# Kernel optimization log

Hardware: AMD Instinct MI355X
Metric: run time of the kernel (lower is better)

## Reference

```python
import jax, jax.numpy as jnp
import numpy as np

N_NODES = 16384
N_GRAPHS = 64
NODES_PER_GRAPH = N_NODES // N_GRAPHS
F_IN = 128
E_DIM = 256
N_HEADS = 8
MLP = 1024
N_LAYERS = 4
N_CLASSES = 10
N_EDGES = 262144
LN_EPS = 1e-5


def setup_inputs() -> dict:
    key = jax.random.key(0)
    ks = jax.random.split(key, 32)
    s = 0.02
    inp = {
        "x": jax.random.normal(ks[0], (N_NODES, F_IN), jnp.float32),
        "edge_idx": jax.random.randint(ks[1], (2, N_EDGES), 0, N_NODES, jnp.int32),
        "batch": (jnp.arange(N_NODES, dtype=jnp.int32) // NODES_PER_GRAPH),
        "pos_enc": jax.random.normal(ks[2], (N_NODES, E_DIM), jnp.float32),
        # GCNConv params (torch Linear convention: W is [out, in])
        "gcn_w": jax.random.normal(ks[3], (F_IN, F_IN), jnp.float32) * s,
        "gcn_b": jnp.zeros((F_IN,), jnp.float32),
        "cls": jax.random.normal(ks[4], (E_DIM,), jnp.float32),
        "emb_w": jax.random.normal(ks[5], (E_DIM, F_IN), jnp.float32) * s,
        "emb_b": jnp.zeros((E_DIM,), jnp.float32),
        # stacked transformer-encoder-layer params over L layers
        "in_w": jax.random.normal(ks[6], (N_LAYERS, 3 * E_DIM, E_DIM), jnp.float32) * s,
        "in_b": jnp.zeros((N_LAYERS, 3 * E_DIM), jnp.float32),
        "out_w": jax.random.normal(ks[7], (N_LAYERS, E_DIM, E_DIM), jnp.float32) * s,
        "out_b": jnp.zeros((N_LAYERS, E_DIM), jnp.float32),
        "lin1_w": jax.random.normal(ks[8], (N_LAYERS, MLP, E_DIM), jnp.float32) * s,
        "lin1_b": jnp.zeros((N_LAYERS, MLP), jnp.float32),
        "lin2_w": jax.random.normal(ks[9], (N_LAYERS, E_DIM, MLP), jnp.float32) * s,
        "lin2_b": jnp.zeros((N_LAYERS, E_DIM), jnp.float32),
        "ln1_g": jnp.ones((N_LAYERS, E_DIM), jnp.float32),
        "ln1_beta": jnp.zeros((N_LAYERS, E_DIM), jnp.float32),
        "ln2_g": jnp.ones((N_LAYERS, E_DIM), jnp.float32),
        "ln2_beta": jnp.zeros((N_LAYERS, E_DIM), jnp.float32),
        "fc_w": jax.random.normal(ks[10], (N_CLASSES, E_DIM), jnp.float32) * s,
        "fc_b": jnp.zeros((N_CLASSES,), jnp.float32),
    }
    return inp


def _layer_norm(h, g, b):
    mu = jnp.mean(h, axis=-1, keepdims=True)
    var = jnp.mean(jnp.square(h - mu), axis=-1, keepdims=True)
    return (h - mu) * jax.lax.rsqrt(var + LN_EPS) * g + b


def _gcn_conv(x, edge_idx, gcn_w, gcn_b):
    # PyG GCNConv: lin -> add self-loops -> sym-normalized scatter-add -> +bias
    xw = x @ gcn_w.T                                             # [N, F]
    ar = jnp.arange(N_NODES, dtype=edge_idx.dtype)
    ei = jnp.concatenate([edge_idx, jnp.stack([ar, ar])], axis=1)
    row, col = ei[0], ei[1]
    deg = jax.ops.segment_sum(jnp.ones(ei.shape[1], xw.dtype), col, num_segments=N_NODES)
    dinv = jax.lax.rsqrt(deg)                                    # deg >= 1 (self loops)
    norm = dinv[row] * dinv[col]                                 # [E+N]
    out = jax.ops.segment_sum(norm[:, None] * xw[row], col, num_segments=N_NODES)
    return out + gcn_b


def reference(x, edge_idx, batch, pos_enc, gcn_w, gcn_b, cls, emb_w, emb_b,
              in_w, in_b, out_w, out_b, lin1_w, lin1_b, lin2_w, lin2_b,
              ln1_g, ln1_beta, ln2_g, ln2_beta, fc_w, fc_b):
    h = _gcn_conv(x, edge_idx, gcn_w, gcn_b)
    h = jax.nn.relu(h)
    h = h @ emb_w.T + emb_b + pos_enc                            # [N, E_DIM]
    # batch = arange // NODES_PER_GRAPH (contiguous equal-size graphs):
    # per-graph loop == batched reshape
    h = h.reshape(N_GRAPHS, NODES_PER_GRAPH, E_DIM)
    cls_tok = jnp.broadcast_to(cls, (N_GRAPHS, 1, E_DIM))
    h = jnp.concatenate([cls_tok, h], axis=1)                    # [G, S, E]
    S = NODES_PER_GRAPH + 1
    dh = E_DIM // N_HEADS
    scale = 1.0 / jnp.sqrt(jnp.asarray(dh, h.dtype))
    for l in range(N_LAYERS):
        # post-LN TransformerEncoderLayer (torch default), dropout off
        qkv = jnp.einsum('gse,fe->gsf', h, in_w[l]) + in_b[l]    # [G, S, 3E]
        q, k, v = jnp.split(qkv, 3, axis=-1)
        q = q.reshape(N_GRAPHS, S, N_HEADS, dh).transpose(0, 2, 1, 3)
        k = k.reshape(N_GRAPHS, S, N_HEADS, dh).transpose(0, 2, 1, 3)
        v = v.reshape(N_GRAPHS, S, N_HEADS, dh).transpose(0, 2, 1, 3)
        att = jax.nn.softmax(jnp.einsum('ghqd,ghkd->ghqk', q, k) * scale, axis=-1)
        o = jnp.einsum('ghqk,ghkd->ghqd', att, v)
        o = o.transpose(0, 2, 1, 3).reshape(N_GRAPHS, S, E_DIM)
        o = jnp.einsum('gse,fe->gsf', o, out_w[l]) + out_b[l]
        h = _layer_norm(h + o, ln1_g[l], ln1_beta[l])
        f = jax.nn.relu(jnp.einsum('gse,me->gsm', h, lin1_w[l]) + lin1_b[l])
        f = jnp.einsum('gsm,em->gse', f, lin2_w[l]) + lin2_b[l]
        h = _layer_norm(h + f, ln2_g[l], ln2_beta[l])
    cls_out = h[:, 0, :]                                         # [G, E]
    return cls_out @ fc_w.T + fc_b                               # [G, C]
```

## Files before the change

kernel.cpp:

```cpp
#include <hip/hip_runtime.h>
#include <cstddef>

#define N_NODES 16384
#define N_GRAPHS 64
#define NPG 256
#define F_IN 128
#define E_DIM 256
#define N_HEADS 8
#define DH 32
#define MLP 1024
#define N_LAYERS 4
#define N_CLASSES 10
#define N_EDGES 262144
#define S_LEN 257
#define M_ROWS (N_GRAPHS * S_LEN)
#define M_PAD 16512
#define LN_EPS 1e-5f

typedef __attribute__((ext_vector_type(8))) short bf16x8;
typedef __attribute__((ext_vector_type(4))) float f32x4;

__device__ inline unsigned short f2b1(float f) {
    unsigned u = __float_as_uint(f);
    unsigned r = (u + 0x7fffu + ((u >> 16) & 1u)) >> 16;
    return (unsigned short)r;
}

#define GLOBAL_LOAD_LDS16(g, l) \
    __builtin_amdgcn_global_load_lds((__attribute__((address_space(1))) const void*)(g), \
                                     (__attribute__((address_space(3))) void*)(l), 16, 0, 0)

struct F2BJobs {
    const float* src[7];
    unsigned short* dst[7];
    int n4[7];
};
__global__ __launch_bounds__(256) void f2b_all(F2BJobs jobs) {
#pragma unroll 1
    for (int r = 0; r < 7; ++r) {
        const float4* s = (const float4*)jobs.src[r];
        ushort4* d = (ushort4*)jobs.dst[r];
        const int n4 = jobs.n4[r];
        for (int i = blockIdx.x * 256 + threadIdx.x; i < n4; i += gridDim.x * 256) {
            float4 v = s[i];
            ushort4 o;
            o.x = f2b1(v.x); o.y = f2b1(v.y); o.z = f2b1(v.z); o.w = f2b1(v.w);
            d[i] = o;
        }
    }
}

__global__ __launch_bounds__(256) void gemm_mfma(
    const unsigned short* __restrict__ A, const unsigned short* __restrict__ W,
    const float* __restrict__ bias, const float* __restrict__ add,
    float* __restrict__ outF, unsigned short* __restrict__ outB,
    int M, int N, int K, int relu)
{
    __shared__ __align__(16) unsigned short As[128 * 32];
    __shared__ __align__(16) unsigned short Bs[128 * 32];
    const int tid = threadIdx.x;
    const int wave = tid >> 6;
    const int lane = tid & 63;
    const int bm = blockIdx.y * 128;
    const int bn = blockIdx.x * 128;

    const int srow = (lane >> 2);
    const int scol = (lane & 3) * 8;
    const size_t a_r0 = (size_t)(bm + wave * 16 + srow) * K + scol;
    const size_t b_r0 = (size_t)(bn + wave * 16 + srow) * K + scol;
    unsigned short* ldsA0 = &As[wave * 512];
    unsigned short* ldsA1 = &As[(wave + 4) * 512];
    unsigned short* ldsB0 = &Bs[wave * 512];
    unsigned short* ldsB1 = &Bs[(wave + 4) * 512];

    const int wm = (wave & 1) * 64;
    const int wn = (wave >> 1) * 64;
    const int fr = lane & 15;
    const int fk = (lane >> 4) * 8;

    f32x4 acc[4][4];
#pragma unroll
    for (int i = 0; i < 4; ++i)
#pragma unroll
        for (int j = 0; j < 4; ++j)
            acc[i][j] = (f32x4){0.f, 0.f, 0.f, 0.f};

    for (int k0 = 0; k0 < K; k0 += 32) {
        __syncthreads();
        GLOBAL_LOAD_LDS16(A + a_r0 + k0, ldsA0);
        GLOBAL_LOAD_LDS16(A + a_r0 + (size_t)64 * K + k0, ldsA1);
        GLOBAL_LOAD_LDS16(W + b_r0 + k0, ldsB0);
        GLOBAL_LOAD_LDS16(W + b_r0 + (size_t)64 * K + k0, ldsB1);
        __syncthreads();

        bf16x8 a[4], b[4];
#pragma unroll
        for (int i = 0; i < 4; ++i)
            a[i] = *(const bf16x8*)&As[(wm + i * 16 + fr) * 32 + fk];
#pragma unroll
        for (int j = 0; j < 4; ++j)
            b[j] = *(const bf16x8*)&Bs[(wn + j * 16 + fr) * 32 + fk];
#pragma unroll
        for (int i = 0; i < 4; ++i)
#pragma unroll
            for (int j = 0; j < 4; ++j)
                acc[i][j] = __builtin_amdgcn_mfma_f32_16x16x32_bf16(a[i], b[j], acc[i][j], 0, 0, 0);
    }

    const int er = (lane >> 4) * 4;
    const int ec = lane & 15;
#pragma unroll
    for (int j = 0; j < 4; ++j) {
        const int col = bn + wn + j * 16 + ec;
        const float bs = bias ? bias[col] : 0.f;
#pragma unroll
        for (int i = 0; i < 4; ++i) {
#pragma unroll
            for (int r = 0; r < 4; ++r) {
                const int row = bm + wm + i * 16 + er + r;
                float v = acc[i][j][r] + bs;
                if (add)  v += add[(size_t)row * N + col];
                if (relu) v = fmaxf(v, 0.f);
                if (outF) outF[(size_t)row * N + col] = v;
                if (outB) outB[(size_t)row * N + col] = f2b1(v);
            }
        }
    }
}

__global__ __launch_bounds__(256) void gemm_ln(
    const unsigned short* __restrict__ A, const unsigned short* __restrict__ W,
    const float* __restrict__ bias, const float* __restrict__ g,
    const float* __restrict__ beta,
    float* __restrict__ h, unsigned short* __restrict__ hb, int K)
{
    __shared__ __align__(16) unsigned short As[64 * 32];
    __shared__ __align__(16) unsigned short Bs[256 * 32];
    const int tid  = threadIdx.x;
    const int wave = tid >> 6;
    const int lane = tid & 63;
    const int quad = lane >> 4;
    const int l16  = lane & 15;
    const int bm   = blockIdx.x * 64;

    const int srow = lane >> 2;
    const int scol = (lane & 3) * 8;
    const size_t a_r0 = (size_t)(bm + wave * 16 + srow) * K + scol;
    unsigned short* ldsA = &As[wave * 512];

    f32x4 acc[16];
#pragma unroll
    for (int j = 0; j < 16; ++j) acc[j] = (f32x4){0.f, 0.f, 0.f, 0.f};

    for (int k0 = 0; k0 < K; k0 += 32) {
        __syncthreads();
        GLOBAL_LOAD_LDS16(A + a_r0 + k0, ldsA);
#pragma unroll
        for (int cc = 0; cc < 4; ++cc) {
            const int c = wave + cc * 4;
            GLOBAL_LOAD_LDS16(W + (size_t)(c * 16 + srow) * K + scol + k0, &Bs[c * 512]);
        }
        __syncthreads();
        bf16x8 a = *(const bf16x8*)&As[(wave * 16 + l16) * 32 + quad * 8];
#pragma unroll
        for (int j = 0; j < 16; ++j) {
            bf16x8 b = *(const bf16x8*)&Bs[(j * 16 + l16) * 32 + quad * 8];
            acc[j] = __builtin_amdgcn_mfma_f32_16x16x32_bf16(a, b, acc[j], 0, 0, 0);
        }
    }

    const int row0 = bm + wave * 16 + quad * 4;
    float gv[16], bv[16], biasv[16];
#pragma unroll
    for (int j = 0; j < 16; ++j) {
        const int col = j * 16 + l16;
        gv[j] = g[col]; bv[j] = beta[col]; biasv[j] = bias[col];
    }
#pragma unroll
    for (int r = 0; r < 4; ++r) {
        const int row = row0 + r;
        float v[16];
        float s1 = 0.f, s2 = 0.f;
#pragma unroll
        for (int j = 0; j < 16; ++j) {
            const int col = j * 16 + l16;
            float t = acc[j][r] + biasv[j] + h[(size_t)row * E_DIM + col];
            v[j] = t; s1 += t; s2 += t * t;
        }
        s1 += __shfl_xor(s1, 1, 64); s2 += __shfl_xor(s2, 1, 64);
        s1 += __shfl_xor(s1, 2, 64); s2 += __shfl_xor(s2, 2, 64);
        s1 += __shfl_xor(s1, 4, 64); s2 += __shfl_xor(s2, 4, 64);
        s1 += __shfl_xor(s1, 8, 64); s2 += __shfl_xor(s2, 8, 64);
        const float mu = s1 * (1.f / 256.f);
        const float var = s2 * (1.f / 256.f) - mu * mu;
        const float rstd = rsqrtf(var + LN_EPS);
#pragma unroll
        for (int j = 0; j < 16; ++j) {
            const int col = j * 16 + l16;
            float o = (v[j] - mu) * rstd * gv[j] + bv[j];
            h[(size_t)row * E_DIM + col] = o;
            hb[(size_t)row * E_DIM + col] = f2b1(o);
        }
    }
}

__global__ void deg_count(const int* __restrict__ ei, float* __restrict__ deg) {
    int e = blockIdx.x * blockDim.x + threadIdx.x;
    if (e < N_EDGES) atomicAdd(&deg[ei[N_EDGES + e]], 1.0f);
}

__global__ __launch_bounds__(1024) void scan_deg(const float* __restrict__ deg,
                                                 int* __restrict__ row_start) {
    __shared__ int lds[1024];
    const int t = threadIdx.x;
    const int base = t * 16;
    int loc[16];
    int s = 0;
#pragma unroll
    for (int i = 0; i < 16; ++i) { loc[i] = s; s += (int)deg[base + i]; }
    lds[t] = s;
    __syncthreads();
    for (int off = 1; off < 1024; off <<= 1) {
        int v = lds[t];
        int u = (t >= off) ? lds[t - off] : 0;
        __syncthreads();
        lds[t] = v + u;
        __syncthreads();
    }
    const int excl = (t == 0) ? 0 : lds[t - 1];
#pragma unroll
    for (int i = 0; i < 16; ++i) row_start[base + i] = excl + loc[i];
    if (t == 1023) row_start[16384] = lds[1023];
}

__global__ void make_dinv(float* __restrict__ deg) {
    int i = blockIdx.x * blockDim.x + threadIdx.x;
    if (i < N_NODES) deg[i] = rsqrtf(deg[i] + 1.0f);
}

__global__ void scatter_edges(const int* __restrict__ ei, const float* __restrict__ dinv,
                              const int* __restrict__ row_start, int* __restrict__ cursor,
                              int* __restrict__ esrc, float* __restrict__ enrm) {
    int e = blockIdx.x * 256 + threadIdx.x;
    if (e < N_EDGES) {
        int r = ei[e], c = ei[N_EDGES + e];
        int slot = atomicAdd(&cursor[c], 1);
        int p = row_start[c] + slot;
        esrc[p] = r;
        enrm[p] = dinv[r] * dinv[c];
    }
}

__global__ __launch_bounds__(256) void gcn_gather(
    const float* __restrict__ xw, const int* __restrict__ row_start,
    const int* __restrict__ esrc, const float* __restrict__ enrm,
    const float* __restrict__ dinv, const float* __restrict__ bias,
    unsigned short* __restrict__ aggb) {
    const int n = blockIdx.x * 4 + (threadIdx.x >> 6);
    const int t = threadIdx.x & 63;
    const int e0 = row_start[n], e1 = row_start[n + 1];
    float ax = 0.f, ay = 0.f;
    for (int e = e0; e < e1; ++e) {
        int s = esrc[e];
        float w = enrm[e];
        float2 v = ((const float2*)(xw + (size_t)s * F_IN))[t];
        ax += w * v.x; ay += w * v.y;
    }
    const float di = dinv[n];
    const float w0 = di * di;
    float2 vs = ((const float2*)(xw + (size_t)n * F_IN))[t];
    ax += w0 * vs.x; ay += w0 * vs.y;
    float2 b2 = ((const float2*)bias)[t];
    ushort2 o;
    o.x = f2b1(fmaxf(ax + b2.x, 0.f));
    o.y = f2b1(fmaxf(ay + b2.y, 0.f));
    ((ushort2*)(aggb + (size_t)n * F_IN))[t] = o;
}

__global__ void assemble_h(const float* __restrict__ emb, const float* __restrict__ cls,
                           float* __restrict__ h, unsigned short* __restrict__ hb) {
    int row = blockIdx.x;
    int f = threadIdx.x;
    int g = row / S_LEN, s = row % S_LEN;
    float v = (s == 0) ? cls[f] : emb[((size_t)g * NPG + (s - 1)) * E_DIM + f];
    h[(size_t)row * E_DIM + f] = v;
    hb[(size_t)row * E_DIM + f] = f2b1(v);
}

__global__ __launch_bounds__(256) void attn_mfma(const unsigned short* __restrict__ qkvb,
                                                 unsigned short* __restrict__ ob) {
    const int g  = blockIdx.x >> 3;
    const int hh = blockIdx.x & 7;
    __shared__ __align__(16) unsigned short Ks[272 * 32];
    __shared__ __align__(16) unsigned short VT[32 * 288];
    __shared__ __align__(16) unsigned short Ps[4 * 16 * 288];
    const int tid  = threadIdx.x;
    const int wave = tid >> 6;
    const int lane = tid & 63;
    const int quad = lane >> 4;
    const int l16  = lane & 15;
    const size_t grow0 = (size_t)g * S_LEN;

    for (int s = tid; s < 272; s += 256) {
        uint4* dst = (uint4*)&Ks[s * 32];
        if (s < S_LEN) {
            const uint4* src = (const uint4*)(qkvb + (grow0 + s) * 768 + 256 + hh * 32);
            dst[0] = src[0]; dst[1] = src[1]; dst[2] = src[2]; dst[3] = src[3];
        } else {
            uint4 z = {0u, 0u, 0u, 0u};
            dst[0] = z; dst[1] = z; dst[2] = z; dst[3] = z;
        }
    }
    for (int s = tid; s < 288; s += 256) {
        unsigned short t[32];
        if (s < S_LEN) {
            const uint4* src = (const uint4*)(qkvb + (grow0 + s) * 768 + 512 + hh * 32);
            ((uint4*)t)[0] = src[0]; ((uint4*)t)[1] = src[1];
            ((uint4*)t)[2] = src[2]; ((uint4*)t)[3] = src[3];
        } else {
#pragma unroll
            for (int d = 0; d < 32; ++d) t[d] = 0;
        }
#pragma unroll
        for (int d = 0; d < 32; ++d) VT[d * 288 + s] = t[d];
    }
    unsigned short* Pw = &Ps[wave * 16 * 288];
    for (int i = lane; i < 256; i += 64)
        Pw[(i >> 4) * 288 + 272 + (i & 15)] = 0;
    __syncthreads();

    const float scale = 0.17677669529663687f;
    for (int qt = wave; qt < 17; qt += 4) {
        const int qrow_l = qt * 16 + l16;
        bf16x8 aq = *(const bf16x8*)(qkvb + (grow0 + qrow_l) * 768 + hh * 32 + quad * 8);

        f32x4 sc[17];
#pragma unroll
        for (int kt = 0; kt < 17; ++kt) {
            bf16x8 bk = *(const bf16x8*)&Ks[(kt * 16 + l16) * 32 + quad * 8];
            f32x4 z = (f32x4){0.f, 0.f, 0.f, 0.f};
            sc[kt] = __builtin_amdgcn_mfma_f32_16x16x32_bf16(aq, bk, z, 0, 0, 0);
        }

        float lsum[4] = {0.f, 0.f, 0.f, 0.f};
#pragma unroll
        for (int kt = 0; kt < 17; ++kt) {
#pragma unroll
            for (int r = 0; r < 4; ++r) {
                float p = __expf(sc[kt][r] * scale);
                if (kt == 16 && l16 != 0) p = 0.f;
                lsum[r] += p;
                Pw[(quad * 4 + r) * 288 + kt * 16 + l16] = f2b1(p);
            }
        }
#pragma unroll
        for (int r = 0; r < 4; ++r) {
            float s = lsum[r];
            s += __shfl_xor(s, 1, 64);
            s += __shfl_xor(s, 2, 64);
            s += __shfl_xor(s, 4, 64);
            s += __shfl_xor(s, 8, 64);
            lsum[r] = s;
        }

        f32x4 o0 = (f32x4){0.f, 0.f, 0.f, 0.f};
        f32x4 o1 = (f32x4){0.f, 0.f, 0.f, 0.f};
#pragma unroll
        for (int c = 0; c < 9; ++c) {
            bf16x8 ap  = *(const bf16x8*)&Pw[l16 * 288 + c * 32 + quad * 8];
            bf16x8 bv0 = *(const bf16x8*)&VT[l16 * 288 + c * 32 + quad * 8];
            bf16x8 bv1 = *(const bf16x8*)&VT[(16 + l16) * 288 + c * 32 + quad * 8];
            o0 = __builtin_amdgcn_mfma_f32_16x16x32_bf16(ap, bv0, o0, 0, 0, 0);
            o1 = __builtin_amdgcn_mfma_f32_16x16x32_bf16(ap, bv1, o1, 0, 0, 0);
        }

#pragma unroll
        for (int r = 0; r < 4; ++r) {
            int row_l = qt * 16 + quad * 4 + r;
            if (row_l < S_LEN) {
                float inv = 1.f / lsum[r];
                size_t orow = (grow0 + row_l) * E_DIM + hh * 32;
                ob[orow + l16]      = f2b1(o0[r] * inv);
                ob[orow + 16 + l16] = f2b1(o1[r] * inv);
            }
        }
    }
}

__global__ void fc_kernel(const float* __restrict__ h, const float* __restrict__ w,
                          const float* __restrict__ b, float* __restrict__ out) {
    int g = blockIdx.x;
    __shared__ float row[E_DIM];
    int t = threadIdx.x;
    row[t] = h[(size_t)g * S_LEN * E_DIM + t];
    __syncthreads();
    if (t < N_CLASSES) {
        float s = 0.f;
        for (int j = 0; j < E_DIM; ++j) s += row[j] * w[t * E_DIM + j];
        out[g * N_CLASSES + t] = s + b[t];
    }
}

extern "C" void kernel_launch(void* const* d_in, const int* in_sizes, int n_in,
                              void* d_out, int out_size, void* d_ws, size_t ws_size,
                              hipStream_t stream) {
    const float* x       = (const float*)d_in[0];
    const int*   edgei   = (const int*)  d_in[1];
    const float* pos_enc = (const float*)d_in[3];
    const float* gcn_w   = (const float*)d_in[4];
    const float* gcn_b   = (const float*)d_in[5];
    const float* cls     = (const float*)d_in[6];
    const float* emb_w   = (const float*)d_in[7];
    const float* emb_b   = (const float*)d_in[8];
    const float* in_w    = (const float*)d_in[9];
    const float* in_b    = (const float*)d_in[10];
    const float* out_w   = (const float*)d_in[11];
    const float* out_b   = (const float*)d_in[12];
    const float* lin1_w  = (const float*)d_in[13];
    const float* lin1_b  = (const float*)d_in[14];
    const float* lin2_w  = (const float*)d_in[15];
    const float* lin2_b  = (const float*)d_in[16];
    const float* ln1_g   = (const float*)d_in[17];
    const float* ln1_be  = (const float*)d_in[18];
    const float* ln2_g   = (const float*)d_in[19];
    const float* ln2_be  = (const float*)d_in[20];
    const float* fc_w    = (const float*)d_in[21];
    const float* fc_b    = (const float*)d_in[22];
    float* out = (float*)d_out;

    float* ws = (float*)d_ws;
    float* h    = ws;
    float* qkv  = h   + (size_t)M_PAD * E_DIM;
    float* xw   = qkv + (size_t)M_PAD * 768;
    float* deg  = xw  + (size_t)N_NODES * F_IN;
    int*   cursor    = (int*)(deg + N_NODES);
    int*   row_start = cursor + N_NODES;
    int*   esrc      = row_start + N_NODES + 1;
    float* enrm      = (float*)(esrc + N_EDGES);
    unsigned short* ub     = (unsigned short*)(enrm + N_EDGES);
    unsigned short* hb     = ub;
    unsigned short* attnob = hb     + (size_t)M_PAD * E_DIM;
    unsigned short* fbufb  = attnob + (size_t)M_PAD * E_DIM;
    unsigned short* xb     = fbufb  + (size_t)M_PAD * MLP;
    unsigned short* aggb   = xb     + (size_t)N_NODES * F_IN;
    unsigned short* gcn_wb = aggb   + (size_t)N_NODES * F_IN;
    unsigned short* emb_wb = gcn_wb + (size_t)F_IN * F_IN;
    unsigned short* in_wb  = emb_wb + (size_t)E_DIM * F_IN;
    unsigned short* out_wb = in_wb  + (size_t)N_LAYERS * 768 * E_DIM;
    unsigned short* lin1_wb= out_wb + (size_t)N_LAYERS * E_DIM * E_DIM;
    unsigned short* lin2_wb= lin1_wb+ (size_t)N_LAYERS * MLP * E_DIM;
    float* emb_out = qkv;
    unsigned short* qkvb = (unsigned short*)qkv;

    F2BJobs jobs;
    jobs.src[0] = x;      jobs.dst[0] = xb;      jobs.n4[0] = N_NODES * F_IN / 4;
    jobs.src[1] = gcn_w;  jobs.dst[1] = gcn_wb;  jobs.n4[1] = F_IN * F_IN / 4;
    jobs.src[2] = emb_w;  jobs.dst[2] = emb_wb;  jobs.n4[2] = E_DIM * F_IN / 4;
    jobs.src[3] = in_w;   jobs.dst[3] = in_wb;   jobs.n4[3] = N_LAYERS * 768 * E_DIM / 4;
    jobs.src[4] = out_w;  jobs.dst[4] = out_wb;  jobs.n4[4] = N_LAYERS * E_DIM * E_DIM / 4;
    jobs.src[5] = lin1_w; jobs.dst[5] = lin1_wb; jobs.n4[5] = N_LAYERS * MLP * E_DIM / 4;
    jobs.src[6] = lin2_w; jobs.dst[6] = lin2_wb; jobs.n4[6] = N_LAYERS * E_DIM * MLP / 4;
    f2b_all<<<1024, 256, 0, stream>>>(jobs);

    hipMemsetAsync(deg, 0, 2 * N_NODES * sizeof(float), stream);
    deg_count<<<(N_EDGES + 255) / 256, 256, 0, stream>>>(edgei, deg);
    scan_deg<<<1, 1024, 0, stream>>>(deg, row_start);
    make_dinv<<<(N_NODES + 255) / 256, 256, 0, stream>>>(deg);
    gemm_mfma<<<dim3(F_IN / 128, N_NODES / 128), 256, 0, stream>>>(
        xb, gcn_wb, nullptr, nullptr, xw, nullptr, N_NODES, F_IN, F_IN, 0);
    scatter_edges<<<(N_EDGES + 255) / 256, 256, 0, stream>>>(edgei, deg, row_start, cursor, esrc, enrm);
    gcn_gather<<<N_NODES / 4, 256, 0, stream>>>(xw, row_start, esrc, enrm, deg, gcn_b, aggb);

    gemm_mfma<<<dim3(E_DIM / 128, N_NODES / 128), 256, 0, stream>>>(
        aggb, emb_wb, emb_b, pos_enc, emb_out, nullptr, N_NODES, E_DIM, F_IN, 0);
    assemble_h<<<M_ROWS, E_DIM, 0, stream>>>(emb_out, cls, h, hb);

    for (int l = 0; l < N_LAYERS; ++l) {
        gemm_mfma<<<dim3(768 / 128, M_PAD / 128), 256, 0, stream>>>(
            hb, in_wb + (size_t)l * 768 * E_DIM, in_b + (size_t)l * 768, nullptr,
            nullptr, qkvb, M_PAD, 768, E_DIM, 0);
        attn_mfma<<<N_GRAPHS * N_HEADS, 256, 0, stream>>>(qkvb, attnob);
        gemm_ln<<<M_PAD / 64, 256, 0, stream>>>(
            attnob, out_wb + (size_t)l * E_DIM * E_DIM, out_b + (size_t)l * E_DIM,
            ln1_g + l * E_DIM, ln1_be + l * E_DIM, h, hb, E_DIM);
        gemm_mfma<<<dim3(MLP / 128, M_PAD / 128), 256, 0, stream>>>(
            hb, lin1_wb + (size_t)l * MLP * E_DIM, lin1_b + (size_t)l * MLP, nullptr,
            nullptr, fbufb, M_PAD, MLP, E_DIM, 1);
        gemm_ln<<<M_PAD / 64, 256, 0, stream>>>(
            fbufb, lin2_wb + (size_t)l * E_DIM * MLP, lin2_b + (size_t)l * E_DIM,
            ln2_g + l * E_DIM, ln2_be + l * E_DIM, h, hb, MLP);
    }

    fc_kernel<<<N_GRAPHS, E_DIM, 0, stream>>>(h, fc_w, fc_b, out);
}
```

Measured before the change: 889.9 us.

## Double-buffer LDS in GEMM kernels and halve gemm_ln row tile

Both GEMM kernels now use two LDS buffers, so the global-to-LDS load for the next K step is issued before the MFMA work on the current one. This halves the barriers per K step and overlaps memory latency with compute. gemm_ln also drops from 64 to 32 rows per block, splitting the 256 output columns across two waves and combining LayerNorm partial sums through shared memory. That doubles the grid for better occupancy, at the cost of more LDS and an extra barrier.

```diff
diff --git a/kernel.cpp b/kernel.cpp
--- a/kernel.cpp
+++ b/kernel.cpp
@@ -56,8 +56,8 @@
     float* __restrict__ outF, unsigned short* __restrict__ outB,
     int M, int N, int K, int relu)
 {
-    __shared__ __align__(16) unsigned short As[128 * 32];
-    __shared__ __align__(16) unsigned short Bs[128 * 32];
+    __shared__ __align__(16) unsigned short As0[128 * 32], As1[128 * 32];
+    __shared__ __align__(16) unsigned short Bs0[128 * 32], Bs1[128 * 32];
     const int tid = threadIdx.x;
     const int wave = tid >> 6;
     const int lane = tid & 63;
@@ -68,10 +68,6 @@
     const int scol = (lane & 3) * 8;
     const size_t a_r0 = (size_t)(bm + wave * 16 + srow) * K + scol;
     const size_t b_r0 = (size_t)(bn + wave * 16 + srow) * K + scol;
-    unsigned short* ldsA0 = &As[wave * 512];
-    unsigned short* ldsA1 = &As[(wave + 4) * 512];
-    unsigned short* ldsB0 = &Bs[wave * 512];
-    unsigned short* ldsB1 = &Bs[(wave + 4) * 512];
 
     const int wm = (wave & 1) * 64;
     const int wn = (wave >> 1) * 64;
@@ -85,26 +81,35 @@
         for (int j = 0; j < 4; ++j)
             acc[i][j] = (f32x4){0.f, 0.f, 0.f, 0.f};
 
-    for (int k0 = 0; k0 < K; k0 += 32) {
-        __syncthreads();
-        GLOBAL_LOAD_LDS16(A + a_r0 + k0, ldsA0);
-        GLOBAL_LOAD_LDS16(A + a_r0 + (size_t)64 * K + k0, ldsA1);
-        GLOBAL_LOAD_LDS16(W + b_r0 + k0, ldsB0);
-        GLOBAL_LOAD_LDS16(W + b_r0 + (size_t)64 * K + k0, ldsB1);
-        __syncthreads();
-
+    auto stage = [&](unsigned short* Asb, unsigned short* Bsb, int k0) {
+        GLOBAL_LOAD_LDS16(A + a_r0 + k0, Asb + wave * 512);
+        GLOBAL_LOAD_LDS16(A + a_r0 + (size_t)64 * K + k0, Asb + (wave + 4) * 512);
+        GLOBAL_LOAD_LDS16(W + b_r0 + k0, Bsb + wave * 512);
+        GLOBAL_LOAD_LDS16(W + b_r0 + (size_t)64 * K + k0, Bsb + (wave + 4) * 512);
+    };
+    auto compute = [&](const unsigned short* Asb, const unsigned short* Bsb) {
         bf16x8 a[4], b[4];
 #pragma unroll
         for (int i = 0; i < 4; ++i)
-            a[i] = *(const bf16x8*)&As[(wm + i * 16 + fr) * 32 + fk];
+            a[i] = *(const bf16x8*)(Asb + (wm + i * 16 + fr) * 32 + fk);
 #pragma unroll
         for (int j = 0; j < 4; ++j)
-            b[j] = *(const bf16x8*)&Bs[(wn + j * 16 + fr) * 32 + fk];
+            b[j] = *(const bf16x8*)(Bsb + (wn + j * 16 + fr) * 32 + fk);
 #pragma unroll
         for (int i = 0; i < 4; ++i)
 #pragma unroll
             for (int j = 0; j < 4; ++j)
                 acc[i][j] = __builtin_amdgcn_mfma_f32_16x16x32_bf16(a[i], b[j], acc[i][j], 0, 0, 0);
+    };
+
+    stage(As0, Bs0, 0);
+    for (int k0 = 0; k0 < K; k0 += 64) {
+        __syncthreads();
+        if (k0 + 32 < K) stage(As1, Bs1, k0 + 32);
+        compute(As0, Bs0);
+        __syncthreads();
+        if (k0 + 64 < K) stage(As0, Bs0, k0 + 64);
+        compute(As1, Bs1);
     }
 
     const int er = (lane >> 4) * 4;
@@ -134,70 +139,90 @@
     const float* __restrict__ beta,
     float* __restrict__ h, unsigned short* __restrict__ hb, int K)
 {
-    __shared__ __align__(16) unsigned short As[64 * 32];
-    __shared__ __align__(16) unsigned short Bs[256 * 32];
+    __shared__ __align__(16) unsigned short As0[32 * 32], As1[32 * 32];
+    __shared__ __align__(16) unsigned short Bs0[256 * 32], Bs1[256 * 32];
+    __shared__ float red[2][2][16][2];
     const int tid  = threadIdx.x;
     const int wave = tid >> 6;
     const int lane = tid & 63;
     const int quad = lane >> 4;
     const int l16  = lane & 15;
-    const int bm   = blockIdx.x * 64;
+    const int rgrp = wave >> 1;
+    const int ch   = wave & 1;
+    const int bm   = blockIdx.x * 32;
 
     const int srow = lane >> 2;
     const int scol = (lane & 3) * 8;
-    const size_t a_r0 = (size_t)(bm + wave * 16 + srow) * K + scol;
-    unsigned short* ldsA = &As[wave * 512];
-
-    f32x4 acc[16];
-#pragma unroll
-    for (int j = 0; j < 16; ++j) acc[j] = (f32x4){0.f, 0.f, 0.f, 0.f};
-
-    for (int k0 = 0; k0 < K; k0 += 32) {
-        __syncthreads();
-        GLOBAL_LOAD_LDS16(A + a_r0 + k0, ldsA);
+
+    f32x4 acc[8];
+#pragma unroll
+    for (int j = 0; j < 8; ++j) acc[j] = (f32x4){0.f, 0.f, 0.f, 0.f};
+
+    auto stage = [&](unsigned short* Asb, unsigned short* Bsb, int k0) {
+        if (wave < 2)
+            GLOBAL_LOAD_LDS16(A + (size_t)(bm + wave * 16 + srow) * K + k0 + scol,
+                              Asb + wave * 512);
 #pragma unroll
         for (int cc = 0; cc < 4; ++cc) {
             const int c = wave + cc * 4;
-            GLOBAL_LOAD_LDS16(W + (size_t)(c * 16 + srow) * K + scol + k0, &Bs[c * 512]);
-        }
+            GLOBAL_LOAD_LDS16(W + (size_t)(c * 16 + srow) * K + k0 + scol, Bsb + c * 512);
+        }
+    };
+    auto compute = [&](const unsigned short* Asb, const unsigned short* Bsb) {
+        bf16x8 a = *(const bf16x8*)(Asb + (rgrp * 16 + l16) * 32 + quad * 8);
+#pragma unroll
+        for (int j = 0; j < 8; ++j) {
+            bf16x8 b = *(const bf16x8*)(Bsb + (ch * 128 + j * 16 + l16) * 32 + quad * 8);
+            acc[j] = __builtin_amdgcn_mfma_f32_16x16x32_bf16(a, b, acc[j], 0, 0, 0);
+        }
+    };
+
+    stage(As0, Bs0, 0);
+    for (int k0 = 0; k0 < K; k0 += 64) {
         __syncthreads();
-        bf16x8 a = *(const bf16x8*)&As[(wave * 16 + l16) * 32 + quad * 8];
-#pragma unroll
-        for (int j = 0; j < 16; ++j) {
-            bf16x8 b = *(const bf16x8*)&Bs[(j * 16 + l16) * 32 + quad * 8];
-            acc[j] = __builtin_amdgcn_mfma_f32_16x16x32_bf16(a, b, acc[j], 0, 0, 0);
-        }
-    }
-
-    const int row0 = bm + wave * 16 + quad * 4;
-    float gv[16], bv[16], biasv[16];
-#pragma unroll
-    for (int j = 0; j < 16; ++j) {
-        const int col = j * 16 + l16;
+        if (k0 + 32 < K) stage(As1, Bs1, k0 + 32);
+        compute(As0, Bs0);
+        __syncthreads();
+        if (k0 + 64 < K) stage(As0, Bs0, k0 + 64);
+        compute(As1, Bs1);
+    }
+
+    float gv[8], bv[8], biasv[8];
+#pragma unroll
+    for (int j = 0; j < 8; ++j) {
+        const int col = ch * 128 + j * 16 + l16;
         gv[j] = g[col]; bv[j] = beta[col]; biasv[j] = bias[col];
     }
+    float v[4][8];
 #pragma unroll
     for (int r = 0; r < 4; ++r) {
-        const int row = row0 + r;
-        float v[16];
+        const int row = bm + rgrp * 16 + quad * 4 + r;
         float s1 = 0.f, s2 = 0.f;
 #pragma unroll
-        for (int j = 0; j < 16; ++j) {
-            const int col = j * 16 + l16;
+        for (int j = 0; j < 8; ++j) {
+            const int col = ch * 128 + j * 16 + l16;
             float t = acc[j][r] + biasv[j] + h[(size_t)row * E_DIM + col];
-            v[j] = t; s1 += t; s2 += t * t;
+            v[r][j] = t; s1 += t; s2 += t * t;
         }
         s1 += __shfl_xor(s1, 1, 64); s2 += __shfl_xor(s2, 1, 64);
         s1 += __shfl_xor(s1, 2, 64); s2 += __shfl_xor(s2, 2, 64);
         s1 += __shfl_xor(s1, 4, 64); s2 += __shfl_xor(s2, 4, 64);
         s1 += __shfl_xor(s1, 8, 64); s2 += __shfl_xor(s2, 8, 64);
-        const float mu = s1 * (1.f / 256.f);
-        const float var = s2 * (1.f / 256.f) - mu * mu;
+        if (l16 == 0) { red[rgrp][ch][quad * 4 + r][0] = s1; red[rgrp][ch][quad * 4 + r][1] = s2; }
+    }
+    __syncthreads();
+#pragma unroll
+    for (int r = 0; r < 4; ++r) {
+        const int row = bm + rgrp * 16 + quad * 4 + r;
+        const float t1 = red[rgrp][0][quad * 4 + r][0] + red[rgrp][1][quad * 4 + r][0];
+        const float t2 = red[rgrp][0][quad * 4 + r][1] + red[rgrp][1][quad * 4 + r][1];
+        const float mu = t1 * (1.f / 256.f);
+        const float var = t2 * (1.f / 256.f) - mu * mu;
         const float rstd = rsqrtf(var + LN_EPS);
 #pragma unroll
-        for (int j = 0; j < 16; ++j) {
-            const int col = j * 16 + l16;
-            float o = (v[j] - mu) * rstd * gv[j] + bv[j];
+        for (int j = 0; j < 8; ++j) {
+            const int col = ch * 128 + j * 16 + l16;
+            float o = (v[r][j] - mu) * rstd * gv[j] + bv[j];
             h[(size_t)row * E_DIM + col] = o;
             hb[(size_t)row * E_DIM + col] = f2b1(o);
         }
@@ -480,13 +505,13 @@
             hb, in_wb + (size_t)l * 768 * E_DIM, in_b + (size_t)l * 768, nullptr,
             nullptr, qkvb, M_PAD, 768, E_DIM, 0);
         attn_mfma<<<N_GRAPHS * N_HEADS, 256, 0, stream>>>(qkvb, attnob);
-        gemm_ln<<<M_PAD / 64, 256, 0, stream>>>(
+        gemm_ln<<<M_PAD / 32, 256, 0, stream>>>(
             attnob, out_wb + (size_t)l * E_DIM * E_DIM, out_b + (size_t)l * E_DIM,
             ln1_g + l * E_DIM, ln1_be + l * E_DIM, h, hb, E_DIM);
         gemm_mfma<<<dim3(MLP / 128, M_PAD / 128), 256, 0, stream>>>(
             hb, lin1_wb + (size_t)l * MLP * E_DIM, lin1_b + (size_t)l * MLP, nullptr,
             nullptr, fbufb, M_PAD, MLP, E_DIM, 1);
-        gemm_ln<<<M_PAD / 64, 256, 0, stream>>>(
+        gemm_ln<<<M_PAD / 32, 256, 0, stream>>>(
             fbufb, lin2_wb + (size_t)l * E_DIM * MLP, lin2_b + (size_t)l * E_DIM,
             ln2_g + l * E_DIM, ln2_be + l * E_DIM, h, hb, MLP);
     }
```

Measured after the change: 871.0 us. -2.1%, faster.
